# Performance work log

Measured on AMD Instinct MI355X. Metric: run time of the kernel, lower is better.

Reference implementation:

```python
import jax, jax.numpy as jnp
import numpy as np
import math

EMBED = 1024
HEADS = 16
HEAD_DIM = EMBED // HEADS
B, Hh, Ww = 256, 10, 10
MAX_POS = 100


def setup_inputs() -> dict:
    key = jax.random.key(0)
    ks = jax.random.split(key, 10)
    s = 1.0 / math.sqrt(EMBED)
    return {
        "x": jax.random.normal(ks[0], (B, EMBED, Hh, Ww), dtype=jnp.float32),
        "Wq": jax.random.uniform(ks[1], (EMBED, EMBED), jnp.float32, -s, s),
        "bq": jax.random.uniform(ks[2], (EMBED,), jnp.float32, -s, s),
        "Wk": jax.random.uniform(ks[3], (EMBED, EMBED), jnp.float32, -s, s),
        "bk": jax.random.uniform(ks[4], (EMBED,), jnp.float32, -s, s),
        "Wv": jax.random.uniform(ks[5], (EMBED, EMBED), jnp.float32, -s, s),
        "bv": jax.random.uniform(ks[6], (EMBED,), jnp.float32, -s, s),
        "Wo": jax.random.uniform(ks[7], (EMBED, EMBED), jnp.float32, -s, s),
        "bo": jax.random.uniform(ks[8], (EMBED,), jnp.float32, -s, s),
        "pos_encoding": jax.random.normal(ks[9], (MAX_POS, EMBED), dtype=jnp.float32),
    }


def reference(x, Wq, bq, Wk, bk, Wv, bv, Wo, bo, pos_encoding):
    # x: [B, E, H, W]
    b, e, h, w = x.shape
    s = h * w  # seq_len
    scale = math.sqrt(HEAD_DIM)
    x_flat = x.reshape(b, e, s).transpose(0, 2, 1)  # [B, S, E]
    x_flat = x_flat + pos_encoding[:s][None]  # broadcast over batch
    q = x_flat @ Wq + bq
    k = x_flat @ Wk + bk
    v = x_flat @ Wv + bv
    # [B, H, S, D]
    q = q.reshape(b, s, HEADS, HEAD_DIM).transpose(0, 2, 1, 3)
    k = k.reshape(b, s, HEADS, HEAD_DIM).transpose(0, 2, 1, 3)
    v = v.reshape(b, s, HEADS, HEAD_DIM).transpose(0, 2, 1, 3)
    scores = jnp.einsum('bhqd,bhkd->bhqk', q, k) / scale
    attn = jax.nn.softmax(scores, axis=-1)  # dropout = identity (eval)
    attended = jnp.einsum('bhqk,bhkd->bhqd', attn, v)
    attended = attended.transpose(0, 2, 1, 3).reshape(b, s, e)
    out = attended @ Wo + bo
    out = out.transpose(0, 2, 1).reshape(b, e, h, w)
    return out, attn
```

## Files before the change

### kernel.cpp

```cpp
#include <hip/hip_runtime.h>

typedef unsigned short u16;
typedef __attribute__((ext_vector_type(8))) short short8;
typedef __attribute__((ext_vector_type(4))) float f32x4;

#define BATCH 256
#define S_LEN 100
#define EMB   1024
#define NHEAD 16
#define HDIM  64

__device__ __forceinline__ float b2f(u16 h) {
  union { unsigned u; float f; } v; v.u = ((unsigned)h) << 16; return v.f;
}
__device__ __forceinline__ u16 f2bf(float f) {
  union { float f; unsigned u; } v; v.f = f;
  unsigned r = v.u + 0x7fffu + ((v.u >> 16) & 1u);
  return (u16)(r >> 16);
}

__device__ __forceinline__ void gld_lds16(const u16* g, u16* l) {
  __builtin_amdgcn_global_load_lds((const __attribute__((address_space(1))) void*)g,
                                   (__attribute__((address_space(3))) void*)l,
                                   16, 0, 0);
}

#define MFMA16(a, b, c) __builtin_amdgcn_mfma_f32_16x16x32_bf16(a, b, c, 0, 0, 0)

__global__ __launch_bounds__(256) void w_xpose(
    const float* __restrict__ Wq, const float* __restrict__ Wk,
    const float* __restrict__ Wv, const float* __restrict__ Wo,
    u16* __restrict__ WtQ, u16* __restrict__ WtK,
    u16* __restrict__ WtV, u16* __restrict__ WtO)
{
  __shared__ u16 tile[64 * 73];
  int z = blockIdx.z;
  const float* W = (z == 0) ? Wq : (z == 1) ? Wk : (z == 2) ? Wv : Wo;
  u16* Wt        = (z == 0) ? WtQ : (z == 1) ? WtK : (z == 2) ? WtV : WtO;
  int k0 = blockIdx.x * 64, n0 = blockIdx.y * 64;
  for (int idx = threadIdx.x; idx < 4096; idx += 256) {
    int r = idx >> 6, c = idx & 63;
    tile[r * 73 + c] = f2bf(W[(size_t)(k0 + r) * EMB + n0 + c]);
  }
  __syncthreads();
  for (int idx = threadIdx.x; idx < 4096; idx += 256) {
    int c = idx >> 6, r = idx & 63;
    Wt[(size_t)(n0 + c) * EMB + k0 + r] = tile[r * 73 + c];
  }
}

__global__ __launch_bounds__(256) void xpose_pos(
    const float* __restrict__ x, const float* __restrict__ pos, u16* __restrict__ xT)
{
  __shared__ float tile[64 * 105];
  int e0 = blockIdx.x * 64;
  int b  = blockIdx.y;
  const float* xb = x + (size_t)b * EMB * S_LEN;
  for (int idx = threadIdx.x; idx < 6400; idx += 256) {
    int i = idx / 100, s = idx - i * 100;
    tile[i * 105 + s] = xb[(size_t)(e0 + i) * S_LEN + s];
  }
  __syncthreads();
  for (int idx = threadIdx.x; idx < 6400; idx += 256) {
    int s = idx >> 6, i = idx & 63;
    float v = tile[i * 105 + s] + pos[(size_t)s * EMB + e0 + i];
    xT[(size_t)b * (S_LEN * EMB) + (size_t)s * EMB + e0 + i] = f2bf(v);
  }
}

__global__ __launch_bounds__(256) void out_xpose(
    const u16* __restrict__ tmp, float* __restrict__ out)
{
  __shared__ u16 tile[100 * 73];
  int e0 = blockIdx.x * 64;
  int b  = blockIdx.y;
  for (int idx = threadIdx.x; idx < 6400; idx += 256) {
    int s = idx >> 6, i = idx & 63;
    tile[s * 73 + i] = tmp[(size_t)b * (S_LEN * EMB) + (size_t)s * EMB + e0 + i];
  }
  __syncthreads();
  for (int idx = threadIdx.x; idx < 6400; idx += 256) {
    int i = idx / 100, s = idx - i * 100;
    out[((size_t)b * EMB + e0 + i) * S_LEN + s] = b2f(tile[s * 73 + i]);
  }
}

__global__ __launch_bounds__(512) void gemm256(
    const u16* __restrict__ A,
    const u16* __restrict__ Bt0, const u16* __restrict__ Bt1, const u16* __restrict__ Bt2,
    const float* __restrict__ bias0, const float* __restrict__ bias1, const float* __restrict__ bias2,
    u16* __restrict__ C0, u16* __restrict__ C1, u16* __restrict__ C2)
{
  __shared__ u16 lds[2][2][16384];

  const int z = blockIdx.z;
  const u16* Bt     = (z == 0) ? Bt0 : (z == 1) ? Bt1 : Bt2;
  const float* bias = (z == 0) ? bias0 : (z == 1) ? bias1 : bias2;
  u16* C            = (z == 0) ? C0 : (z == 1) ? C1 : C2;

  const int tid  = threadIdx.x;
  const int wave = tid >> 6, lane = tid & 63;
  const int quad = lane >> 4, l16 = lane & 15;
  const int m0 = blockIdx.x * 256, n0 = blockIdx.y * 256;
  const int WM = (wave >> 2) * 128, WN = (wave & 3) * 64;

  const int rq8  = tid >> 3;
  const int jg   = ((tid & 7) ^ (rq8 & 7)) << 3;
  const int hi96 = (tid >= 256) ? 96 : 0;
  const int aw   = (wave & 3) * 8 + (wave >> 2) * 128;
  const size_t aBase = (size_t)(m0 + rq8 + hi96) * EMB + jg;
  const size_t bBase = (size_t)(n0 + rq8) * EMB + jg;

#define STB(nb, u, k1) gld_lds16(Bt + bBase + (size_t)((u) * 64) * EMB + (k1), \
                                 &lds[nb][1][(u) * 4096 + wave * 512])
#define STA(nb, p, k1) gld_lds16(A + aBase + (size_t)((p) * 32) * EMB + (k1), \
                                 &lds[nb][0][((p) * 32 + aw) * 64])
#define GATE(N) { asm volatile("s_waitcnt vmcnt(" #N ")" ::: "memory"); \
                  __builtin_amdgcn_s_barrier(); }

  f32x4 acc[8][4] = {};

  STB(0, 0, 0); STB(0, 1, 0); STB(0, 2, 0); STB(0, 3, 0);
  STA(0, 0, 0); STA(0, 1, 0); STA(0, 2, 0); STA(0, 3, 0);
  GATE(3);

  const int swz = l16 & 7;
  const int cA  = (quad ^ swz) << 3;
  const int cB  = ((quad + 4) ^ swz) << 3;

#define PH(q, STAGES, GATE_) { \
    short8 aF[2][2]; \
    aF[0][0] = *(const short8*)(a0 + (2 * (q)) * 1024); \
    aF[0][1] = *(const short8*)(a1 + (2 * (q)) * 1024); \
    aF[1][0] = *(const short8*)(a0 + (2 * (q) + 1) * 1024); \
    aF[1][1] = *(const short8*)(a1 + (2 * (q) + 1) * 1024); \
    STAGES; \
    __builtin_amdgcn_s_setprio(1); \
    _Pragma("unroll") \
    for (int kh = 0; kh < 2; ++kh) { \
      _Pragma("unroll") \
      for (int ni = 0; ni < 4; ++ni) { \
        acc[2 * (q)][ni]     = MFMA16(aF[0][kh], bF[kh][ni], acc[2 * (q)][ni]); \
        acc[2 * (q) + 1][ni] = MFMA16(aF[1][kh], bF[kh][ni], acc[2 * (q) + 1][ni]); \
      } \
    } \
    __builtin_amdgcn_s_setprio(0); \
    GATE_; \
  }

  for (int t = 0; t < 16; ++t) {
    const int cb = t & 1, nb = cb ^ 1;
    const u16* lA_ = lds[cb][0];
    const u16* lB_ = lds[cb][1];
    const u16* a0 = lA_ + (WM + l16) * 64 + cA;
    const u16* a1 = lA_ + (WM + l16) * 64 + cB;
    const u16* b0 = lB_ + (WN + l16) * 64 + cA;
    const u16* b1 = lB_ + (WN + l16) * 64 + cB;
    const int k1 = (t + 1) << 6;

    short8 bF[2][4];
#pragma unroll
    for (int ni = 0; ni < 4; ++ni) {
      bF[0][ni] = *(const short8*)(b0 + ni * 1024);
      bF[1][ni] = *(const short8*)(b1 + ni * 1024);
    }

    if (t < 15) {
      PH(0, { STB(nb, 0, k1); STB(nb, 1, k1); }, GATE(4));
      PH(1, { STB(nb, 2, k1); STB(nb, 3, k1); }, GATE(5));
      PH(2, { STA(nb, 0, k1); STA(nb, 1, k1); }, GATE(6));
      PH(3, { STA(nb, 2, k1); STA(nb, 3, k1); }, GATE(3));
    } else {
      PH(0, { (void)0; }, GATE(2));
      PH(1, { (void)0; }, GATE(1));
      PH(2, { (void)0; }, GATE(0));
      PH(3, { (void)0; }, { (void)0; });
    }
  }

#pragma unroll
  for (int ni = 0; ni < 4; ++ni) {
    int col = n0 + WN + ni * 16 + l16;
    float bv = bias[col];
#pragma unroll
    for (int mi = 0; mi < 8; ++mi) {
#pragma unroll
      for (int r = 0; r < 4; ++r) {
        int row = m0 + WM + mi * 16 + quad * 4 + r;
        C[(size_t)row * EMB + col] = f2bf(acc[mi][ni][r] + bv);
      }
    }
  }
#undef PH
#undef STB
#undef STA
#undef GATE
}

__global__ __launch_bounds__(256) void attn_kernel(
    const u16* __restrict__ Q, const u16* __restrict__ Kb, const u16* __restrict__ V,
    float* __restrict__ attn_out, u16* __restrict__ attended)
{
  __shared__ u16 sQK[112 * 64 * 2];
  __shared__ __align__(16) char smemB[100 * 105 * 4];
  __shared__ float sRed[256];

  u16* sQ   = sQK;
  u16* sK   = sQK + 112 * 64;
  u16* sP   = sQK;
  float* sS = (float*)smemB;
  u16* sVt  = (u16*)smemB;

  const int bh = blockIdx.x;
  const int b = bh >> 4, h = bh & 15;
  const int tid = threadIdx.x;
  const int wave = tid >> 6, lane = tid & 63;
  const int quad = lane >> 4, l16 = lane & 15;
  const size_t qbase = (size_t)b * S_LEN * EMB + h * HDIM;

  uint4 vr0, vr1, vr2, vr3 = make_uint4(0, 0, 0, 0);
  {
    int c0 = tid, c1 = tid + 256, c2 = tid + 512;
    vr0 = *(const uint4*)(V + qbase + (size_t)(c0 >> 3) * EMB + ((c0 & 7) << 3));
    vr1 = *(const uint4*)(V + qbase + (size_t)(c1 >> 3) * EMB + ((c1 & 7) << 3));
    vr2 = *(const uint4*)(V + qbase + (size_t)(c2 >> 3) * EMB + ((c2 & 7) << 3));
    if (tid < 32) {
      int c3 = tid + 768;
      vr3 = *(const uint4*)(V + qbase + (size_t)(c3 >> 3) * EMB + ((c3 & 7) << 3));
    }
  }

  for (int c = tid; c < 896; c += 256) {
    int s = c >> 3, j = c & 7;
    int jg = (j ^ (s & 7)) << 3;
    uint4 qv = make_uint4(0, 0, 0, 0), kv = make_uint4(0, 0, 0, 0);
    if (s < S_LEN) {
      qv = *(const uint4*)(Q  + qbase + (size_t)s * EMB + jg);
      kv = *(const uint4*)(Kb + qbase + (size_t)s * EMB + jg);
    }
    *(uint4*)(sQ + c * 8) = qv;
    *(uint4*)(sK + c * 8) = kv;
  }
  __syncthreads();

  for (int t = wave; t < 49; t += 4) {
    int mi = t / 7, ni = t - mi * 7;
    f32x4 acc = {0.f, 0.f, 0.f, 0.f};
#pragma unroll
    for (int kk = 0; kk < 64; kk += 32) {
      int rq = mi * 16 + l16, rk = ni * 16 + l16;
      int cix = (kk >> 3) + quad;
      short8 a  = *(const short8*)(sQ + rq * 64 + ((cix ^ (rq & 7)) << 3));
      short8 bb = *(const short8*)(sK + rk * 64 + ((cix ^ (rk & 7)) << 3));
      acc = __builtin_amdgcn_mfma_f32_16x16x32_bf16(a, bb, acc, 0, 0, 0);
    }
    int col = ni * 16 + l16;
#pragma unroll
    for (int r = 0; r < 4; ++r) {
      int row = mi * 16 + quad * 4 + r;
      if (row < S_LEN && col < S_LEN) sS[row * 105 + col] = acc[r] * 0.125f;
    }
  }
  __syncthreads();

  for (int i = tid; i < 192; i += 256)
    *(uint4*)(sP + (100 + (i >> 4)) * 128 + ((i & 15) << 3)) = make_uint4(0, 0, 0, 0);

  if (tid < 200) {
    int row = tid >> 1, half = tid & 1;
    float* Srow = sS + row * 105;
    int c0 = half * 50, c1 = c0 + 50;
    float m0 = -1e30f, m1 = -1e30f;
    for (int c = c0; c < c1; c += 2) {
      m0 = fmaxf(m0, Srow[c]);
      m1 = fmaxf(m1, Srow[c + 1]);
    }
    sRed[tid] = fmaxf(m0, m1);
  }
  __syncthreads();
  if (tid < 200) {
    int row = tid >> 1, half = tid & 1;
    float* Srow = sS + row * 105;
    float mxv = fmaxf(sRed[row * 2], sRed[row * 2 + 1]);
    int c0 = half * 50, c1 = c0 + 50;
    float s0 = 0.f, s1 = 0.f;
    for (int c = c0; c < c1; c += 2) {
      float e0 = __expf(Srow[c] - mxv);
      float e1 = __expf(Srow[c + 1] - mxv);
      Srow[c] = e0; Srow[c + 1] = e1;
      s0 += e0; s1 += e1;
    }
    sRed[tid] = s0 + s1;
  }
  __syncthreads();
  if (tid < 200) {
    int row = tid >> 1, half = tid & 1;
    float* Srow = sS + row * 105;
    u16* Prow = sP + row * 128;
    int rs = row & 7;
    float inv = 1.f / (sRed[row * 2] + sRed[row * 2 + 1]);
    int c0 = half * 50, c1 = c0 + 50;
    for (int c = c0; c < c1; ++c) {
      float p = Srow[c] * inv;
      Srow[c] = p;
      Prow[(((c >> 3) ^ rs) << 3) + (c & 7)] = f2bf(p);
    }
    if (half == 1) {
      for (int c = S_LEN; c < 128; ++c)
        Prow[(((c >> 3) ^ rs) << 3) + (c & 7)] = 0;
    }
  }
  __syncthreads();

  {
    float* ao = attn_out + (size_t)bh * (S_LEN * S_LEN);
    for (int i = tid; i < S_LEN * S_LEN; i += 256) {
      int r = i / 100, c = i - r * 100;
      ao[i] = sS[r * 105 + c];
    }
  }
  __syncthreads();

  for (int i = tid; i < 1024; i += 256)
    *(uint4*)(sVt + i * 8) = make_uint4(0, 0, 0, 0);
  __syncthreads();
  {
    const u16* p0 = (const u16*)&vr0;
    const u16* p1 = (const u16*)&vr1;
    const u16* p2 = (const u16*)&vr2;
    const u16* p3 = (const u16*)&vr3;
    int c0 = tid, c1 = tid + 256, c2 = tid + 512, c3 = tid + 768;
#pragma unroll
    for (int j = 0; j < 8; ++j) {
      int s, d;
      s = c0 >> 3; d = ((c0 & 7) << 3) + j;
      sVt[d * 128 + (((s >> 3) ^ (d & 7)) << 3) + (s & 7)] = p0[j];
      s = c1 >> 3; d = ((c1 & 7) << 3) + j;
      sVt[d * 128 + (((s >> 3) ^ (d & 7)) << 3) + (s & 7)] = p1[j];
      s = c2 >> 3; d = ((c2 & 7) << 3) + j;
      sVt[d * 128 + (((s >> 3) ^ (d & 7)) << 3) + (s & 7)] = p2[j];
      if (tid < 32) {
        s = c3 >> 3; d = ((c3 & 7) << 3) + j;
        sVt[d * 128 + (((s >> 3) ^ (d & 7)) << 3) + (s & 7)] = p3[j];
      }
    }
  }
  __syncthreads();

  for (int t = wave; t < 28; t += 4) {
    int mi = t >> 2, ni = t & 3;
    f32x4 acc = {0.f, 0.f, 0.f, 0.f};
#pragma unroll
    for (int kk = 0; kk < 128; kk += 32) {
      int rp = mi * 16 + l16, rv = ni * 16 + l16;
      int cix = (kk >> 3) + quad;
      short8 a  = *(const short8*)(sP  + rp * 128 + ((cix ^ (rp & 7)) << 3));
      short8 bb = *(const short8*)(sVt + rv * 128 + ((cix ^ (rv & 7)) << 3));
      acc = __builtin_amdgcn_mfma_f32_16x16x32_bf16(a, bb, acc, 0, 0, 0);
    }
    int col = ni * 16 + l16;
#pragma unroll
    for (int r = 0; r < 4; ++r) {
      int row = mi * 16 + quad * 4 + r;
      if (row < S_LEN)
        attended[((size_t)b * S_LEN + row) * EMB + h * HDIM + col] = f2bf(acc[r]);
    }
  }
}

extern "C" void kernel_launch(void* const* d_in, const int* in_sizes, int n_in,
                              void* d_out, int out_size, void* d_ws, size_t ws_size,
                              hipStream_t stream) {
  const float* x   = (const float*)d_in[0];
  const float* Wq  = (const float*)d_in[1];
  const float* bq  = (const float*)d_in[2];
  const float* Wk  = (const float*)d_in[3];
  const float* bk  = (const float*)d_in[4];
  const float* Wv  = (const float*)d_in[5];
  const float* bv  = (const float*)d_in[6];
  const float* Wo  = (const float*)d_in[7];
  const float* bo  = (const float*)d_in[8];
  const float* pos = (const float*)d_in[9];

  float* out  = (float*)d_out;
  float* attn = out + (size_t)BATCH * EMB * S_LEN;

  const size_t MTOT = (size_t)BATCH * S_LEN;
  u16* ws   = (u16*)d_ws;
  u16* xT   = ws;
  u16* Qb   = ws + MTOT * EMB;
  u16* Kbuf = ws + 2 * MTOT * EMB;
  u16* Vb   = ws + 3 * MTOT * EMB;
  u16* WtQ  = ws + 4 * MTOT * EMB;
  u16* WtK  = WtQ + (size_t)EMB * EMB;
  u16* WtV  = WtK + (size_t)EMB * EMB;
  u16* WtO  = WtV + (size_t)EMB * EMB;
  u16* attended = xT;
  u16* tmp      = Qb;

  w_xpose<<<dim3(16, 16, 4), 256, 0, stream>>>(Wq, Wk, Wv, Wo, WtQ, WtK, WtV, WtO);
  xpose_pos<<<dim3(16, BATCH), 256, 0, stream>>>(x, pos, xT);
  gemm256<<<dim3(100, 4, 3), 512, 0, stream>>>(xT, WtQ, WtK, WtV, bq, bk, bv,
                                               Qb, Kbuf, Vb);
  attn_kernel<<<dim3(BATCH * NHEAD), 256, 0, stream>>>(Qb, Kbuf, Vb, attn, attended);
  gemm256<<<dim3(100, 4, 1), 512, 0, stream>>>(attended, WtO, WtO, WtO, bo, bo, bo,
                                               tmp, tmp, tmp);
  out_xpose<<<dim3(16, BATCH), 256, 0, stream>>>(tmp, out);
}
```

Measured before the change: 744.8 us.

## Replace double-buffered GEMM staging with five-slot half-tile ring buffer

```diff
diff --git a/kernel.cpp b/kernel.cpp
--- a/kernel.cpp
+++ b/kernel.cpp
@@ -91,7 +91,7 @@
     const float* __restrict__ bias0, const float* __restrict__ bias1, const float* __restrict__ bias2,
     u16* __restrict__ C0, u16* __restrict__ C1, u16* __restrict__ C2)
 {
-  __shared__ u16 lds[2][2][16384];
+  __shared__ u16 lds[5 * 16384];
 
   const int z = blockIdx.z;
   const u16* Bt     = (z == 0) ? Bt0 : (z == 1) ? Bt1 : Bt2;
@@ -104,59 +104,56 @@
   const int m0 = blockIdx.x * 256, n0 = blockIdx.y * 256;
   const int WM = (wave >> 2) * 128, WN = (wave & 3) * 64;
 
-  const int rq8  = tid >> 3;
-  const int jg   = ((tid & 7) ^ (rq8 & 7)) << 3;
-  const int hi96 = (tid >= 256) ? 96 : 0;
-  const int aw   = (wave & 3) * 8 + (wave >> 2) * 128;
-  const size_t aBase = (size_t)(m0 + rq8 + hi96) * EMB + jg;
-  const size_t bBase = (size_t)(n0 + rq8) * EMB + jg;
-
-#define STB(nb, u, k1) gld_lds16(Bt + bBase + (size_t)((u) * 64) * EMB + (k1), \
-                                 &lds[nb][1][(u) * 4096 + wave * 512])
-#define STA(nb, p, k1) gld_lds16(A + aBase + (size_t)((p) * 32) * EMB + (k1), \
-                                 &lds[nb][0][((p) * 32 + aw) * 64])
-#define GATE(N) { asm volatile("s_waitcnt vmcnt(" #N ")" ::: "memory"); \
-                  __builtin_amdgcn_s_barrier(); }
-
-  f32x4 acc[8][4] = {};
-
-  STB(0, 0, 0); STB(0, 1, 0); STB(0, 2, 0); STB(0, 3, 0);
-  STA(0, 0, 0); STA(0, 1, 0); STA(0, 2, 0); STA(0, 3, 0);
-  GATE(3);
+  const int rq64 = tid >> 3;
+  const int jg   = ((tid & 7) ^ (rq64 & 7)) << 3;
 
   const int swz = l16 & 7;
   const int cA  = (quad ^ swz) << 3;
   const int cB  = ((quad + 4) ^ swz) << 3;
-
-#define PH(q, STAGES, GATE_) { \
-    short8 aF[2][2]; \
-    aF[0][0] = *(const short8*)(a0 + (2 * (q)) * 1024); \
-    aF[0][1] = *(const short8*)(a1 + (2 * (q)) * 1024); \
-    aF[1][0] = *(const short8*)(a0 + (2 * (q) + 1) * 1024); \
-    aF[1][1] = *(const short8*)(a1 + (2 * (q) + 1) * 1024); \
-    STAGES; \
-    __builtin_amdgcn_s_setprio(1); \
-    _Pragma("unroll") \
-    for (int kh = 0; kh < 2; ++kh) { \
-      _Pragma("unroll") \
-      for (int ni = 0; ni < 4; ++ni) { \
-        acc[2 * (q)][ni]     = MFMA16(aF[0][kh], bF[kh][ni], acc[2 * (q)][ni]); \
-        acc[2 * (q) + 1][ni] = MFMA16(aF[1][kh], bF[kh][ni], acc[2 * (q) + 1][ni]); \
-      } \
-    } \
-    __builtin_amdgcn_s_setprio(0); \
-    GATE_; \
-  }
-
+  const int wmh = WM >> 7;
+  const int wnh = WN >> 7;
+  const int bRow = (WN & 127) + l16;
+
+#define STAGE_SLOT(s, ri) { \
+    const size_t kof = (size_t)((s) >> 1) * 64 + jg; \
+    const int hof = 128 * ((s) & 1); \
+    u16* dst = lds + (size_t)(ri) * 16384 + tid * 8; \
+    gld_lds16(A  + (size_t)(m0 + hof + rq64)      * EMB + kof, dst); \
+    gld_lds16(A  + (size_t)(m0 + hof + 64 + rq64) * EMB + kof, dst + 4096); \
+    gld_lds16(Bt + (size_t)(n0 + hof + rq64)      * EMB + kof, dst + 8192); \
+    gld_lds16(Bt + (size_t)(n0 + hof + 64 + rq64) * EMB + kof, dst + 12288); \
+  }
+
+  f32x4 acc[8][4] = {};
+
+  STAGE_SLOT(0, 0); STAGE_SLOT(1, 1); STAGE_SLOT(2, 2);
+  STAGE_SLOT(3, 3); STAGE_SLOT(4, 4);
+
+  int ri0 = 0, ri1 = 1;
+#pragma unroll 1
   for (int t = 0; t < 16; ++t) {
-    const int cb = t & 1, nb = cb ^ 1;
-    const u16* lA_ = lds[cb][0];
-    const u16* lB_ = lds[cb][1];
-    const u16* a0 = lA_ + (WM + l16) * 64 + cA;
-    const u16* a1 = lA_ + (WM + l16) * 64 + cB;
-    const u16* b0 = lB_ + (WN + l16) * 64 + cA;
-    const u16* b1 = lB_ + (WN + l16) * 64 + cB;
-    const int k1 = (t + 1) << 6;
+    if (t == 0) {
+      asm volatile("s_waitcnt vmcnt(12)" ::: "memory");
+    } else if (t == 15) {
+      asm volatile("s_waitcnt vmcnt(0)" ::: "memory");
+    } else {
+      asm volatile("s_waitcnt vmcnt(4)" ::: "memory");
+    }
+    __builtin_amdgcn_s_barrier();
+
+    if (t >= 1) {
+      int s1 = 2 * t + 3;
+      if (s1 <= 31) { int ia = ri1 + 2; if (ia >= 5) ia -= 5; STAGE_SLOT(s1, ia); }
+      int s2 = 2 * t + 4;
+      if (s2 <= 31) { int ib = ri1 + 3; if (ib >= 5) ib -= 5; STAGE_SLOT(s2, ib); }
+    }
+
+    const u16* sA = lds + (size_t)(wmh ? ri1 : ri0) * 16384;
+    const u16* sB = lds + (size_t)(wnh ? ri1 : ri0) * 16384 + 8192;
+    const u16* a0 = sA + l16 * 64 + cA;
+    const u16* a1 = sA + l16 * 64 + cB;
+    const u16* b0 = sB + bRow * 64 + cA;
+    const u16* b1 = sB + bRow * 64 + cB;
 
     short8 bF[2][4];
 #pragma unroll
@@ -164,18 +161,27 @@
       bF[0][ni] = *(const short8*)(b0 + ni * 1024);
       bF[1][ni] = *(const short8*)(b1 + ni * 1024);
     }
-
-    if (t < 15) {
-      PH(0, { STB(nb, 0, k1); STB(nb, 1, k1); }, GATE(4));
-      PH(1, { STB(nb, 2, k1); STB(nb, 3, k1); }, GATE(5));
-      PH(2, { STA(nb, 0, k1); STA(nb, 1, k1); }, GATE(6));
-      PH(3, { STA(nb, 2, k1); STA(nb, 3, k1); }, GATE(3));
-    } else {
-      PH(0, { (void)0; }, GATE(2));
-      PH(1, { (void)0; }, GATE(1));
-      PH(2, { (void)0; }, GATE(0));
-      PH(3, { (void)0; }, { (void)0; });
-    }
+    __builtin_amdgcn_s_setprio(1);
+#pragma unroll
+    for (int p = 0; p < 4; ++p) {
+      short8 aF[2][2];
+      aF[0][0] = *(const short8*)(a0 + (2 * p) * 1024);
+      aF[0][1] = *(const short8*)(a1 + (2 * p) * 1024);
+      aF[1][0] = *(const short8*)(a0 + (2 * p + 1) * 1024);
+      aF[1][1] = *(const short8*)(a1 + (2 * p + 1) * 1024);
+#pragma unroll
+      for (int kh = 0; kh < 2; ++kh) {
+#pragma unroll
+        for (int ni = 0; ni < 4; ++ni) {
+          acc[2 * p][ni]     = MFMA16(aF[0][kh], bF[kh][ni], acc[2 * p][ni]);
+          acc[2 * p + 1][ni] = MFMA16(aF[1][kh], bF[kh][ni], acc[2 * p + 1][ni]);
+        }
+      }
+    }
+    __builtin_amdgcn_s_setprio(0);
+
+    ri0 += 2; if (ri0 >= 5) ri0 -= 5;
+    ri1 += 2; if (ri1 >= 5) ri1 -= 5;
   }
 
 #pragma unroll
@@ -191,10 +197,7 @@
       }
     }
   }
-#undef PH
-#undef STB
-#undef STA
-#undef GATE
+#undef STAGE_SLOT
 }
 
 __global__ __launch_bounds__(256) void attn_kernel(
```

After: 771.0 us. +3.5%, slower.
